# Kernel optimization log

Hardware: AMD Instinct MI355X
Metric: run time of the kernel (lower is better)

Reference implementation:

```python
import jax, jax.numpy as jnp
import numpy as np

NUM_RAYS = 524288
NUM_EXISTING = 64   # coarse samples per ray
NUM_SAMPLES = 64    # fine PDF samples -> num_bins = 65
HIST_PAD = 0.01
EPS = 1e-5


def setup_inputs() -> dict:
    key = jax.random.key(0)
    kw, kd = jax.random.split(key)
    weights = jax.random.uniform(kw, (NUM_RAYS, NUM_EXISTING, 1), dtype=jnp.float32)
    # build monotonically increasing per-ray bin edges (near plane ~2.0)
    deltas = jax.random.uniform(kd, (NUM_RAYS, NUM_EXISTING + 1), dtype=jnp.float32,
                                minval=0.01, maxval=0.1)
    edges = 2.0 + jnp.cumsum(deltas, axis=-1)          # [R, N+1]
    starts = edges[..., :-1, None]                      # [R, N, 1]
    ends = edges[..., 1:, None]                         # [R, N, 1]
    return {"weights": weights, "starts": starts, "ends": ends}


def _pdf_sample(weights, starts, ends):
    # weights/starts/ends: [R, N, 1]
    w = weights[..., 0] + HIST_PAD                      # [R, N]
    ws = jnp.sum(w, axis=-1, keepdims=True)             # [R, 1]
    padding = jax.nn.relu(EPS - ws)
    w = w + padding / w.shape[-1]
    ws = ws + padding
    pdf = w / ws
    cdf = jnp.minimum(jnp.ones_like(pdf), jnp.cumsum(pdf, axis=-1))
    cdf = jnp.concatenate([jnp.zeros_like(cdf[..., :1]), cdf], axis=-1)  # [R, N+1]

    num_bins = NUM_SAMPLES + 1
    u = jnp.linspace(0.0, 1.0, num_bins, dtype=cdf.dtype)
    u = jnp.broadcast_to(u, (*cdf.shape[:-1], num_bins))                 # [R, num_bins]

    s = starts[..., 0]
    e = ends[..., 0]
    existing_bins = jnp.concatenate(
        [s[..., :1], (s[..., 1:] + e[..., :-1]) / 2.0, e[..., -1:]], axis=-1)  # [R, N+1]

    inds = jax.vmap(lambda c, uu: jnp.searchsorted(c, uu, side='right'))(cdf, u)
    nmax = existing_bins.shape[-1] - 1
    below = jnp.clip(inds - 1, 0, nmax)
    above = jnp.clip(inds, 0, nmax)
    cdf_g0 = jnp.take_along_axis(cdf, below, axis=-1)
    bins_g0 = jnp.take_along_axis(existing_bins, below, axis=-1)
    cdf_g1 = jnp.take_along_axis(cdf, above, axis=-1)
    bins_g1 = jnp.take_along_axis(existing_bins, above, axis=-1)

    t = jnp.clip(jnp.nan_to_num((u - cdf_g0) / (cdf_g1 - cdf_g0), nan=0.0), 0.0, 1.0)
    bins = bins_g0 + t * (bins_g1 - bins_g0)             # [R, num_bins]
    # include_original=True: merge with existing bins and sort
    bins = jnp.sort(jnp.concatenate([existing_bins, bins], axis=-1), axis=-1)  # [R, 2N+2]
    return bins


def reference(weights, starts, ends):
    bins = _pdf_sample(weights, starts, ends)
    # bin_starts = bins[..., :-1, None], bin_ends = bins[..., 1:, None]
    return bins
```

## Files before the change

kernel.cpp:

```cpp
#include <hip/hip_runtime.h>


#define NUM_RAYS 524288
#define NE 64
#define HIST_PAD 0.01f
#define EPS_PAD 1e-5f

constexpr int WAVES = 4;
constexpr int RPW   = 4;
constexpr int RPB   = WAVES * RPW;
constexpr int BLOCK = WAVES * 64;
constexpr int ROW   = 130;

typedef float f32x4 __attribute__((ext_vector_type(4)));

template <int CTRL, int ROW_MASK = 0xf>
__device__ __forceinline__ float dpp0f(float x) {
    return __int_as_float(
        __builtin_amdgcn_update_dpp(0, __float_as_int(x), CTRL, ROW_MASK, 0xf, true));
}
template <int CTRL, int ROW_MASK = 0xf>
__device__ __forceinline__ int dpp0i(int x) {
    return __builtin_amdgcn_update_dpp(0, x, CTRL, ROW_MASK, 0xf, true);
}

__global__ __launch_bounds__(BLOCK) void pdf_sample_kernel(
    const float* __restrict__ weights,
    const float* __restrict__ starts,
    const float* __restrict__ ends,
    float* __restrict__ out)
{
    __shared__ __align__(16) float s_o[RPB][ROW];

    const int lane = threadIdx.x & 63;
    const int wvid = threadIdx.x >> 6;
    const int ray0 = blockIdx.x * RPB + wvid * RPW;
    const int sub  = lane >> 4;
    const int col  = lane & 15;
    const int k0   = col << 2;

    const f32x4 w4 = ((const f32x4*)(weights + (size_t)ray0 * NE))[lane];
    const f32x4 s4 = ((const f32x4*)(starts  + (size_t)ray0 * NE))[lane];
    const float e_last = ends[(size_t)(ray0 + sub) * NE + 63];

    const float p0 = w4.x + HIST_PAD;
    const float p1 = p0 + (w4.y + HIST_PAD);
    const float p2 = p1 + (w4.z + HIST_PAD);
    const float p3 = p2 + (w4.w + HIST_PAD);

    float x = p3;
    x += dpp0f<0x111>(x);
    x += dpp0f<0x112>(x);
    x += dpp0f<0x114>(x);
    x += dpp0f<0x118>(x);
    const float excl = x - p3;

    const float ws      = __shfl(x, lane | 15, 64);
    const float padding = fmaxf(EPS_PAD - ws, 0.0f);
    float rtot;
    asm("v_rcp_f32 %0, %1" : "=v"(rtot) : "v"(ws + padding));
    const float pad64 = padding * (1.0f / 64.0f);
    const float pk    = (float)k0 * pad64;

    const float cdf0 = fminf((excl + p0 + (pk + 1.0f * pad64)) * rtot, 1.0f);
    const float cdf1 = fminf((excl + p1 + (pk + 2.0f * pad64)) * rtot, 1.0f);
    const float cdf2 = fminf((excl + p2 + (pk + 3.0f * pad64)) * rtot, 1.0f);
    const float cdf3 = fminf((excl + p3 + (pk + 4.0f * pad64)) * rtot, 1.0f);
    const int t0 = (int)ceilf(cdf0 * 64.0f);
    const int t1 = (int)ceilf(cdf1 * 64.0f);
    const int t2 = (int)ceilf(cdf2 * 64.0f);
    const int t3 = (int)ceilf(cdf3 * 64.0f);

    const float cprev = dpp0f<0x111>(cdf3);
    const int   tprev = dpp0i<0x111>(t3);
    float snext = dpp0f<0x101>(s4.x);
    if (col == 15) snext = e_last;

    float* const srow = &s_o[wvid * RPW + sub][0];

    const float cL[4]  = {cprev, cdf0, cdf1, cdf2};
    const float cR[4]  = {cdf0, cdf1, cdf2, cdf3};
    const int   tL[4]  = {tprev, t0, t1, t2};
    const int   tR[4]  = {t0, t1, t2, t3};
    const float bL[4]  = {s4.x, s4.y, s4.z, s4.w};
    const float bR[4]  = {s4.y, s4.z, s4.w, snext};

    #pragma unroll
    for (int j = 0; j < 4; ++j) {
        const int k = k0 + j;
        srow[k + tL[j]] = bL[j];

        const float denom = cR[j] - cL[j];
        float rden;
        asm("v_rcp_f32 %0, %1" : "=v"(rden) : "v"(denom));
        const float slope = (bR[j] - bL[j]) * rden;
        float v = fmaf((float)tL[j], 1.0f / 64.0f, -cL[j]);
        for (int q = tL[j]; q < tR[j]; ++q) {
            srow[q + k + 1] = fmaf(v, slope, bL[j]);
            v += 1.0f / 64.0f;
        }
    }

    if (col == 15) {
        srow[2 * NE + 1] = e_last;
        srow[NE + t3]    = e_last;
        for (int q = t3; q < NE; ++q)
            srow[q + NE + 1] = e_last;
    }

    __syncthreads();

    const f32x4* sf = (const f32x4*)&s_o[0][0];
    f32x4* ob = (f32x4*)(out + (size_t)blockIdx.x * (RPB * ROW));
    const int t = threadIdx.x;
    __builtin_nontemporal_store(sf[t],         &ob[t]);
    __builtin_nontemporal_store(sf[t + BLOCK], &ob[t + BLOCK]);
    if (t < RPB * ROW / 4 - 2 * BLOCK)
        __builtin_nontemporal_store(sf[t + 2 * BLOCK], &ob[t + 2 * BLOCK]);
}

extern "C" void kernel_launch(void* const* d_in, const int* in_sizes, int n_in,
                              void* d_out, int out_size, void* d_ws, size_t ws_size,
                              hipStream_t stream) {
    const float* weights = (const float*)d_in[0];
    const float* starts  = (const float*)d_in[1];
    const float* ends    = (const float*)d_in[2];
    float* out = (float*)d_out;

    const int grid = NUM_RAYS / RPB;
    pdf_sample_kernel<<<grid, BLOCK, 0, stream>>>(weights, starts, ends, out);
}
```

Before: 107.6 us.

## Make kernel persistent with per-wave tiles, prefetch, and double-buffered LDS

```diff
diff --git a/kernel.cpp b/kernel.cpp
--- a/kernel.cpp
+++ b/kernel.cpp
@@ -11,6 +11,8 @@
 constexpr int RPB   = WAVES * RPW;
 constexpr int BLOCK = WAVES * 64;
 constexpr int ROW   = 130;
+constexpr int GRID  = 2048;
+constexpr int TILES = NUM_RAYS / (GRID * RPB);
 
 typedef float f32x4 __attribute__((ext_vector_type(4)));
 
@@ -30,93 +32,108 @@
     const float* __restrict__ ends,
     float* __restrict__ out)
 {
-    __shared__ __align__(16) float s_o[RPB][ROW];
+    __shared__ __align__(16) float s_o[2][WAVES][RPW * ROW];
 
     const int lane = threadIdx.x & 63;
     const int wvid = threadIdx.x >> 6;
-    const int ray0 = blockIdx.x * RPB + wvid * RPW;
     const int sub  = lane >> 4;
     const int col  = lane & 15;
     const int k0   = col << 2;
 
-    const f32x4 w4 = ((const f32x4*)(weights + (size_t)ray0 * NE))[lane];
-    const f32x4 s4 = ((const f32x4*)(starts  + (size_t)ray0 * NE))[lane];
-    const float e_last = ends[(size_t)(ray0 + sub) * NE + 63];
+    const unsigned rbase = (unsigned)blockIdx.x * (TILES * RPB) + (unsigned)(wvid * RPW);
 
-    const float p0 = w4.x + HIST_PAD;
-    const float p1 = p0 + (w4.y + HIST_PAD);
-    const float p2 = p1 + (w4.z + HIST_PAD);
-    const float p3 = p2 + (w4.w + HIST_PAD);
+    unsigned off = rbase * NE;
+    f32x4 w4 = ((const f32x4*)(weights + off))[lane];
+    f32x4 s4 = ((const f32x4*)(starts  + off))[lane];
+    float el = ends[off + (unsigned)(sub * NE) + 63u];
 
-    float x = p3;
-    x += dpp0f<0x111>(x);
-    x += dpp0f<0x112>(x);
-    x += dpp0f<0x114>(x);
-    x += dpp0f<0x118>(x);
-    const float excl = x - p3;
+    for (int t = 0; t < TILES; ++t) {
+        f32x4 w4n, s4n; float eln;
+        if (t + 1 < TILES) {
+            const unsigned offn = (rbase + (unsigned)((t + 1) * RPB)) * NE;
+            w4n = ((const f32x4*)(weights + offn))[lane];
+            s4n = ((const f32x4*)(starts  + offn))[lane];
+            eln = ends[offn + (unsigned)(sub * NE) + 63u];
+        }
 
-    const float ws      = __shfl(x, lane | 15, 64);
-    const float padding = fmaxf(EPS_PAD - ws, 0.0f);
-    float rtot;
-    asm("v_rcp_f32 %0, %1" : "=v"(rtot) : "v"(ws + padding));
-    const float pad64 = padding * (1.0f / 64.0f);
-    const float pk    = (float)k0 * pad64;
+        const float e_last = el;
 
-    const float cdf0 = fminf((excl + p0 + (pk + 1.0f * pad64)) * rtot, 1.0f);
-    const float cdf1 = fminf((excl + p1 + (pk + 2.0f * pad64)) * rtot, 1.0f);
-    const float cdf2 = fminf((excl + p2 + (pk + 3.0f * pad64)) * rtot, 1.0f);
-    const float cdf3 = fminf((excl + p3 + (pk + 4.0f * pad64)) * rtot, 1.0f);
-    const int t0 = (int)ceilf(cdf0 * 64.0f);
-    const int t1 = (int)ceilf(cdf1 * 64.0f);
-    const int t2 = (int)ceilf(cdf2 * 64.0f);
-    const int t3 = (int)ceilf(cdf3 * 64.0f);
+        const float p0 = w4.x + HIST_PAD;
+        const float p1 = p0 + (w4.y + HIST_PAD);
+        const float p2 = p1 + (w4.z + HIST_PAD);
+        const float p3 = p2 + (w4.w + HIST_PAD);
 
-    const float cprev = dpp0f<0x111>(cdf3);
-    const int   tprev = dpp0i<0x111>(t3);
-    float snext = dpp0f<0x101>(s4.x);
-    if (col == 15) snext = e_last;
+        float x = p3;
+        x += dpp0f<0x111>(x);
+        x += dpp0f<0x112>(x);
+        x += dpp0f<0x114>(x);
+        x += dpp0f<0x118>(x);
+        const float excl = x - p3;
 
-    float* const srow = &s_o[wvid * RPW + sub][0];
+        const float ws      = __shfl(x, lane | 15, 64);
+        const float padding = fmaxf(EPS_PAD - ws, 0.0f);
+        float rtot;
+        asm("v_rcp_f32 %0, %1" : "=v"(rtot) : "v"(ws + padding));
+        const float pad64 = padding * (1.0f / 64.0f);
+        const float pk    = (float)k0 * pad64;
 
-    const float cL[4]  = {cprev, cdf0, cdf1, cdf2};
-    const float cR[4]  = {cdf0, cdf1, cdf2, cdf3};
-    const int   tL[4]  = {tprev, t0, t1, t2};
-    const int   tR[4]  = {t0, t1, t2, t3};
-    const float bL[4]  = {s4.x, s4.y, s4.z, s4.w};
-    const float bR[4]  = {s4.y, s4.z, s4.w, snext};
+        const float cdf0 = fminf((excl + p0 + (pk + 1.0f * pad64)) * rtot, 1.0f);
+        const float cdf1 = fminf((excl + p1 + (pk + 2.0f * pad64)) * rtot, 1.0f);
+        const float cdf2 = fminf((excl + p2 + (pk + 3.0f * pad64)) * rtot, 1.0f);
+        const float cdf3 = fminf((excl + p3 + (pk + 4.0f * pad64)) * rtot, 1.0f);
+        const int t0 = (int)ceilf(cdf0 * 64.0f);
+        const int t1 = (int)ceilf(cdf1 * 64.0f);
+        const int t2 = (int)ceilf(cdf2 * 64.0f);
+        const int t3 = (int)ceilf(cdf3 * 64.0f);
 
-    #pragma unroll
-    for (int j = 0; j < 4; ++j) {
-        const int k = k0 + j;
-        srow[k + tL[j]] = bL[j];
+        const float cprev = dpp0f<0x111>(cdf3);
+        const int   tprev = dpp0i<0x111>(t3);
+        float snext = dpp0f<0x101>(s4.x);
+        if (col == 15) snext = e_last;
 
-        const float denom = cR[j] - cL[j];
-        float rden;
-        asm("v_rcp_f32 %0, %1" : "=v"(rden) : "v"(denom));
-        const float slope = (bR[j] - bL[j]) * rden;
-        float v = fmaf((float)tL[j], 1.0f / 64.0f, -cL[j]);
-        for (int q = tL[j]; q < tR[j]; ++q) {
-            srow[q + k + 1] = fmaf(v, slope, bL[j]);
-            v += 1.0f / 64.0f;
+        float* const srow = &s_o[t & 1][wvid][sub * ROW];
+
+        const float cL[4] = {cprev, cdf0, cdf1, cdf2};
+        const float cR[4] = {cdf0, cdf1, cdf2, cdf3};
+        const int   tL[4] = {tprev, t0, t1, t2};
+        const int   tR[4] = {t0, t1, t2, t3};
+        const float bL[4] = {s4.x, s4.y, s4.z, s4.w};
+        const float bR[4] = {s4.y, s4.z, s4.w, snext};
+
+        #pragma unroll
+        for (int j = 0; j < 4; ++j) {
+            const int k = k0 + j;
+            srow[k + tL[j]] = bL[j];
+
+            const float denom = cR[j] - cL[j];
+            float rden;
+            asm("v_rcp_f32 %0, %1" : "=v"(rden) : "v"(denom));
+            const float slope = (bR[j] - bL[j]) * rden;
+            float v = fmaf((float)tL[j], 1.0f / 64.0f, -cL[j]);
+            for (int q = tL[j]; q < tR[j]; ++q) {
+                srow[q + k + 1] = fmaf(v, slope, bL[j]);
+                v += 1.0f / 64.0f;
+            }
         }
+
+        if (col == 15) {
+            srow[2 * NE + 1] = e_last;
+            srow[NE + t3]    = e_last;
+            for (int q = t3; q < NE; ++q)
+                srow[q + NE + 1] = e_last;
+        }
+
+        asm volatile("s_waitcnt lgkmcnt(0)" ::: "memory");
+
+        const f32x4* sf = (const f32x4*)&s_o[t & 1][wvid][0];
+        f32x4* ob = (f32x4*)(out + (size_t)(rbase + (unsigned)(t * RPB)) * ROW);
+        __builtin_nontemporal_store(sf[lane],      &ob[lane]);
+        __builtin_nontemporal_store(sf[lane + 64], &ob[lane + 64]);
+        if (lane < 2)
+            __builtin_nontemporal_store(sf[lane + 128], &ob[lane + 128]);
+
+        w4 = w4n; s4 = s4n; el = eln;
     }
-
-    if (col == 15) {
-        srow[2 * NE + 1] = e_last;
-        srow[NE + t3]    = e_last;
-        for (int q = t3; q < NE; ++q)
-            srow[q + NE + 1] = e_last;
-    }
-
-    __syncthreads();
-
-    const f32x4* sf = (const f32x4*)&s_o[0][0];
-    f32x4* ob = (f32x4*)(out + (size_t)blockIdx.x * (RPB * ROW));
-    const int t = threadIdx.x;
-    __builtin_nontemporal_store(sf[t],         &ob[t]);
-    __builtin_nontemporal_store(sf[t + BLOCK], &ob[t + BLOCK]);
-    if (t < RPB * ROW / 4 - 2 * BLOCK)
-        __builtin_nontemporal_store(sf[t + 2 * BLOCK], &ob[t + 2 * BLOCK]);
 }
 
 extern "C" void kernel_launch(void* const* d_in, const int* in_sizes, int n_in,
@@ -127,6 +144,5 @@
     const float* ends    = (const float*)d_in[2];
     float* out = (float*)d_out;
 
-    const int grid = NUM_RAYS / RPB;
-    pdf_sample_kernel<<<grid, BLOCK, 0, stream>>>(weights, starts, ends, out);
+    pdf_sample_kernel<<<GRID, BLOCK, 0, stream>>>(weights, starts, ends, out);
 }
```

Measured after the change: 128.4 us. 19.3% more time.
